# Kernel optimization log

Measured on AMD Instinct MI355X. Metric: run time of the kernel, lower is better.

## Reference

```python
import jax, jax.numpy as jnp
import numpy as np

N_RAYS = 65536
S_UNIFORM = 256          # 2 * n_samples coarse samples per ray
N_IMP = 128              # importance samples per ray
TRUNCATION = 2.0 / 512.0 * 4.0  # default in sdf2weights


def raw2weights_occupancy(raw):
    # raw2outputs_nerf_color with occupancy=True
    alpha = jax.nn.sigmoid(10.0 * raw)  # [N, S]
    trans = jnp.cumprod(
        jnp.concatenate([jnp.ones_like(alpha[:, :1]), 1.0 - alpha + 1e-10], axis=-1),
        axis=-1,
    )[:, :-1]
    return alpha, alpha * trans


def sample_pdf_det(bins, weights, n_samples):
    # bins: [N, M], weights: [N, M-1]; deterministic (det=True) inverse-CDF sampling
    w = weights + 1e-5
    pdf = w / jnp.sum(w, axis=-1, keepdims=True)
    cdf = jnp.cumsum(pdf, axis=-1)
    cdf = jnp.concatenate([jnp.zeros_like(cdf[..., :1]), cdf], axis=-1)  # [N, M]
    u = jnp.linspace(0.0, 1.0, n_samples, dtype=cdf.dtype)
    u = jnp.broadcast_to(u, cdf.shape[:-1] + (n_samples,))               # [N, n]
    inds = jax.vmap(lambda c, uu: jnp.searchsorted(c, uu, side='right'))(cdf, u)
    below = jnp.maximum(inds - 1, 0)
    above = jnp.minimum(inds, cdf.shape[-1] - 1)
    cdf_b = jnp.take_along_axis(cdf, below, axis=-1)
    cdf_a = jnp.take_along_axis(cdf, above, axis=-1)
    bins_b = jnp.take_along_axis(bins, below, axis=-1)
    bins_a = jnp.take_along_axis(bins, above, axis=-1)
    denom = cdf_a - cdf_b
    denom = jnp.where(denom < 1e-5, jnp.ones_like(denom), denom)
    t = (u - cdf_b) / denom
    return bins_b + t * (bins_a - bins_b)


def sdf2weights(sdf, z_vals, truncation=TRUNCATION, sc_factor=1.0):
    alpha = jax.nn.sigmoid(sdf / truncation) * jax.nn.sigmoid(-sdf / truncation)
    signs = sdf[:, 1:] * sdf[:, :-1]
    sign_mask = jnp.where(signs < 0.0, 1.0, 0.0)
    inds = jnp.argmax(sign_mask, axis=1)[:, None]              # first zero-crossing
    z_min = jnp.take_along_axis(z_vals, inds, axis=1)          # [N, 1]
    trunc_mask = jnp.where(z_vals < z_min + sc_factor * truncation, 1.0, 0.0)
    alpha = alpha * trunc_mask
    weights = alpha / (jnp.sum(alpha, axis=-1, keepdims=True) + 1e-8)
    return weights


def setup_inputs() -> dict:
    key = jax.random.key(0)
    k1, k2, k3, k4 = jax.random.split(key, 4)
    occ = jax.random.normal(k1, (N_RAYS, S_UNIFORM), dtype=jnp.float32)
    # monotonically increasing depths in [0.1, 4.1)
    z_vals_u = jnp.sort(
        jax.random.uniform(k2, (N_RAYS, S_UNIFORM), dtype=jnp.float32) * 4.0 + 0.1,
        axis=-1,
    )
    sdf = jax.random.normal(k3, (N_RAYS, N_IMP), dtype=jnp.float32) * 0.05
    rgbs = jax.random.uniform(k4, (N_RAYS, N_IMP, 3), dtype=jnp.float32)
    return {"occ": occ, "z_vals_u": z_vals_u, "sdf": sdf, "rgbs": rgbs}


def reference(occ, z_vals_u, sdf, rgbs):
    # 1) coarse occupancy compositing -> weights
    _, w_u = raw2weights_occupancy(occ)
    # 2) inverse-CDF importance sampling over midpoints (detached, as in gen_samples)
    z_mid = 0.5 * (z_vals_u[..., 1:] + z_vals_u[..., :-1])
    z_samples = jax.lax.stop_gradient(sample_pdf_det(z_mid, w_u[..., 1:-1], N_IMP))
    # 3) TSDF weights at importance samples
    weights = sdf2weights(sdf, z_samples)
    # 4) composite
    rgb_map = jnp.clip(jnp.sum(weights[..., None] * rgbs, axis=-2), 0.0, 1.0)  # [N,3]
    depth_map = jnp.sum(weights * z_samples, axis=-1)                          # [N]
    return jnp.concatenate([rgb_map, depth_map[:, None], weights], axis=-1)    # [N, 4+N_IMP]
```

## Files before the change

kernel.cpp:

```cpp
#include <hip/hip_runtime.h>

#define S_U 256
#define N_IMP 128
#define OUT_STRIDE (4 + N_IMP)
#define TRUNC 0.015625f
#define WPB 4
#define INV127 (1.0f / 127.0f)

template <int CTRL, int ROWM>
__device__ __forceinline__ float dppf(float identity, float x) {
    return __int_as_float(__builtin_amdgcn_update_dpp(
        __float_as_int(identity), __float_as_int(x), CTRL, ROWM, 0xf, false));
}

__device__ __forceinline__ float wscan_add(float x) {
    x += dppf<0x111, 0xf>(0.f, x);
    x += dppf<0x112, 0xf>(0.f, x);
    x += dppf<0x114, 0xf>(0.f, x);
    x += dppf<0x118, 0xf>(0.f, x);
    x += dppf<0x142, 0xa>(0.f, x);
    x += dppf<0x143, 0xc>(0.f, x);
    return x;
}

__device__ __forceinline__ float wscan_mul(float x) {
    x *= dppf<0x111, 0xf>(1.f, x);
    x *= dppf<0x112, 0xf>(1.f, x);
    x *= dppf<0x114, 0xf>(1.f, x);
    x *= dppf<0x118, 0xf>(1.f, x);
    x *= dppf<0x142, 0xa>(1.f, x);
    x *= dppf<0x143, 0xc>(1.f, x);
    return x;
}

__device__ __forceinline__ int wscan_min(int x) {
    const int I = 0x7fffffff;
    x = min(x, __builtin_amdgcn_update_dpp(I, x, 0x111, 0xf, 0xf, false));
    x = min(x, __builtin_amdgcn_update_dpp(I, x, 0x112, 0xf, 0xf, false));
    x = min(x, __builtin_amdgcn_update_dpp(I, x, 0x114, 0xf, 0xf, false));
    x = min(x, __builtin_amdgcn_update_dpp(I, x, 0x118, 0xf, 0xf, false));
    x = min(x, __builtin_amdgcn_update_dpp(I, x, 0x142, 0xa, 0xf, false));
    x = min(x, __builtin_amdgcn_update_dpp(I, x, 0x143, 0xc, 0xf, false));
    return x;
}

__device__ __forceinline__ int k_of(float c) {
    int k = (int)ceilf(c * 127.0f);
    k = min(max(k, 0), 128);
    if (k > 0 && c <= (float)(k - 1) * INV127) --k;
    else if (k < 128 && !(c <= (float)k * INV127)) ++k;
    return k;
}

__global__ __launch_bounds__(256) void tsdf_render_kernel(
    const float* __restrict__ occ,
    const float* __restrict__ zvals,
    const float* __restrict__ sdf,
    const float* __restrict__ rgbs,
    float* __restrict__ out)
{
    const int lane = threadIdx.x & 63;
    const int wv   = threadIdx.x >> 6;
    const int ray  = blockIdx.x * WPB + wv;

    __shared__ __align__(16) float2 s_pair[WPB][S_U];
    __shared__ int s_below[WPB][N_IMP];

    const float4 o4 = ((const float4*)(occ   + (size_t)ray * S_U))[lane];
    const float4 z4 = ((const float4*)(zvals + (size_t)ray * S_U))[lane];
    const float2 sd2 = ((const float2*)(sdf + (size_t)ray * N_IMP))[lane];
    const float2* rg = (const float2*)(rgbs + (size_t)ray * (N_IMP * 3)) + lane * 3;
    const float2 p0 = rg[0];
    const float2 p1 = rg[1];
    const float2 p2 = rg[2];

    float a0 = 1.0f / (1.0f + __expf(-10.0f * o4.x));
    float a1 = 1.0f / (1.0f + __expf(-10.0f * o4.y));
    float a2 = 1.0f / (1.0f + __expf(-10.0f * o4.z));
    float a3 = 1.0f / (1.0f + __expf(-10.0f * o4.w));
    float t0 = 1.0f - a0 + 1e-10f;
    float t1 = 1.0f - a1 + 1e-10f;
    float t2 = 1.0f - a2 + 1e-10f;
    float t3 = 1.0f - a3 + 1e-10f;
    float pp0 = t0, pp1 = pp0 * t1, pp2 = pp1 * t2, pp3 = pp2 * t3;
    float ip = wscan_mul(pp3);
    float pbase = __shfl_up(ip, 1);
    if (lane == 0) pbase = 1.0f;

    float w0 = a0 * pbase;
    float w1 = a1 * pbase * pp0;
    float w2 = a2 * pbase * pp1;
    float w3 = a3 * pbase * pp2;

    float v0 = (lane > 0)  ? w0 + 1e-5f : 0.0f;
    float v1 = w1 + 1e-5f;
    float v2 = w2 + 1e-5f;
    float v3 = (lane < 63) ? w3 + 1e-5f : 0.0f;
    float s0 = v0, s1 = s0 + v1, s2 = s1 + v2, s3 = s2 + v3;
    float is = wscan_add(s3);
    float total = __shfl(is, 63);
    float sbase = __shfl_up(is, 1);
    if (lane == 0) sbase = 0.0f;
    float invt = 1.0f / total;

    float c0 = (sbase + s0) * invt;
    float c1 = (sbase + s1) * invt;
    float c2 = (sbase + s2) * invt;
    float c3 = (sbase + s3) * invt;

    float znext = __shfl_down(z4.x, 1);
    float zm0 = 0.5f * (z4.x + z4.y);
    float zm1 = 0.5f * (z4.y + z4.z);
    float zm2 = 0.5f * (z4.z + z4.w);
    float zm3 = 0.5f * (z4.w + znext);

    float2* pr = s_pair[wv];
    *(float4*)&pr[lane * 4 + 0] = make_float4(c0, zm0, c1, zm1);
    *(float4*)&pr[lane * 4 + 2] = make_float4(c2, zm2, c3, zm3);

    int k0 = k_of(c0), k1 = k_of(c1), k2 = k_of(c2), k3 = k_of(c3);
    int kn = __shfl_down(k0, 1);
    if (lane == 63) { k3 = 128; kn = 128; }
    int base = lane * 4;
    int* bel = s_below[wv];
    for (int j = k0; j < k1; ++j) bel[j] = base;
    for (int j = k1; j < k2; ++j) bel[j] = base + 1;
    for (int j = k2; j < k3; ++j) bel[j] = base + 2;
    for (int j = k3; j < kn; ++j) bel[j] = base + 3;

    __builtin_amdgcn_wave_barrier();

    int jj0 = 2 * lane, jj1 = 2 * lane + 1;
    int b0 = bel[jj0], b1 = bel[jj1];
    float2 pb0 = pr[b0];
    float2 pa0 = pr[min(b0 + 1, 254)];
    float2 pb1 = pr[b1];
    float2 pa1 = pr[min(b1 + 1, 254)];

    float u0 = (float)jj0 * INV127;
    float u1 = (float)jj1 * INV127;
    float d0 = pa0.x - pb0.x; d0 = (d0 < 1e-5f) ? 1.0f : d0;
    float d1 = pa1.x - pb1.x; d1 = (d1 < 1e-5f) ? 1.0f : d1;
    float zs0 = pb0.y + ((u0 - pb0.x) / d0) * (pa0.y - pb0.y);
    float zs1 = pb1.y + ((u1 - pb1.x) / d1) * (pa1.y - pb1.y);

    float sn = __shfl_down(sd2.x, 1);
    int c = 0x7fffffff;
    if (sd2.x * sd2.y < 0.0f)                 c = 2 * lane;
    else if (lane < 63 && sd2.y * sn < 0.0f)  c = 2 * lane + 1;
    c = wscan_min(c);
    int ci = __shfl(c, 63);
    if (ci == 0x7fffffff) ci = 0;
    float zca = __shfl(zs0, ci >> 1);
    float zcb = __shfl(zs1, ci >> 1);
    float z_min = (ci & 1) ? zcb : zca;

    float x0 = sd2.x * (1.0f / TRUNC);
    float x1 = sd2.y * (1.0f / TRUNC);
    float al0 = 1.0f / (2.0f + __expf(x0) + __expf(-x0));
    float al1 = 1.0f / (2.0f + __expf(x1) + __expf(-x1));
    float zlim = z_min + TRUNC;
    if (!(zs0 < zlim)) al0 = 0.0f;
    if (!(zs1 < zlim)) al1 = 0.0f;

    float sA = wscan_add(al0 + al1);
    float sR = wscan_add(al0 * p0.x + al1 * p1.y);
    float sG = wscan_add(al0 * p0.y + al1 * p2.x);
    float sB = wscan_add(al0 * p1.x + al1 * p2.y);
    float sD = wscan_add(al0 * zs0  + al1 * zs1);

    float asum = __shfl(sA, 63);
    float inv_s = 1.0f / (asum + 1e-8f);

    float* ob = out + (size_t)ray * OUT_STRIDE;
    ((float2*)(ob + 4))[lane] = make_float2(al0 * inv_s, al1 * inv_s);
    if (lane == 63) {
        float inv63 = 1.0f / (sA + 1e-8f);
        ob[0] = fminf(fmaxf(sR * inv63, 0.0f), 1.0f);
        ob[1] = fminf(fmaxf(sG * inv63, 0.0f), 1.0f);
        ob[2] = fminf(fmaxf(sB * inv63, 0.0f), 1.0f);
        ob[3] = sD * inv63;
    }
}

extern "C" void kernel_launch(void* const* d_in, const int* in_sizes, int n_in,
                              void* d_out, int out_size, void* d_ws, size_t ws_size,
                              hipStream_t stream) {
    const float* occ  = (const float*)d_in[0];
    const float* z    = (const float*)d_in[1];
    const float* sdf  = (const float*)d_in[2];
    const float* rgbs = (const float*)d_in[3];
    float* out = (float*)d_out;
    const int n_rays = in_sizes[0] / S_U;
    hipLaunchKernelGGL(tsdf_render_kernel, dim3(n_rays / WPB), dim3(256), 0, stream,
                       occ, z, sdf, rgbs, out);
}
```

Baseline: 269.4 us.

## Replace divergent searchsorted fill loops with merge-path flag scan

Replaces the per-lane variable-length loops that write below-indices for each u sample with a merge-style approach. Each CDF point marks its merged position in a shared flag array, a wave prefix sum over those flags gives ranks, and each lane writes the below index for the u slots it owns. This is meant to remove warp divergence and load imbalance when many samples fall into a few bins. In exchange it adds extra LDS traffic, zeroing work, an integer scan and extra shared memory, which may lower occupancy.

After: 271.1 us. No clear change (+0.6%).

```diff
diff --git a/kernel.cpp b/kernel.cpp
--- a/kernel.cpp
+++ b/kernel.cpp
@@ -6,6 +6,7 @@
 #define TRUNC 0.015625f
 #define WPB 4
 #define INV127 (1.0f / 127.0f)
+#define MERGE_N 384
 
 template <int CTRL, int ROWM>
 __device__ __forceinline__ float dppf(float identity, float x) {
@@ -30,6 +31,16 @@
     x *= dppf<0x118, 0xf>(1.f, x);
     x *= dppf<0x142, 0xa>(1.f, x);
     x *= dppf<0x143, 0xc>(1.f, x);
+    return x;
+}
+
+__device__ __forceinline__ int wscan_add_i(int x) {
+    x += __builtin_amdgcn_update_dpp(0, x, 0x111, 0xf, 0xf, false);
+    x += __builtin_amdgcn_update_dpp(0, x, 0x112, 0xf, 0xf, false);
+    x += __builtin_amdgcn_update_dpp(0, x, 0x114, 0xf, 0xf, false);
+    x += __builtin_amdgcn_update_dpp(0, x, 0x118, 0xf, 0xf, false);
+    x += __builtin_amdgcn_update_dpp(0, x, 0x142, 0xa, 0xf, false);
+    x += __builtin_amdgcn_update_dpp(0, x, 0x143, 0xc, 0xf, false);
     return x;
 }
 
@@ -64,6 +75,7 @@
     const int ray  = blockIdx.x * WPB + wv;
 
     __shared__ __align__(16) float2 s_pair[WPB][S_U];
+    __shared__ __align__(16) int s_A[WPB][MERGE_N];
     __shared__ int s_below[WPB][N_IMP];
 
     const float4 o4 = ((const float4*)(occ   + (size_t)ray * S_U))[lane];
@@ -73,6 +85,10 @@
     const float2 p0 = rg[0];
     const float2 p1 = rg[1];
     const float2 p2 = rg[2];
+
+    int4* Az = (int4*)s_A[wv];
+    Az[lane] = make_int4(0, 0, 0, 0);
+    if (lane < 32) Az[64 + lane] = make_int4(0, 0, 0, 0);
 
     float a0 = 1.0f / (1.0f + __expf(-10.0f * o4.x));
     float a1 = 1.0f / (1.0f + __expf(-10.0f * o4.y));
@@ -119,26 +135,47 @@
     *(float4*)&pr[lane * 4 + 2] = make_float4(c2, zm2, c3, zm3);
 
     int k0 = k_of(c0), k1 = k_of(c1), k2 = k_of(c2), k3 = k_of(c3);
-    int kn = __shfl_down(k0, 1);
-    if (lane == 63) { k3 = 128; kn = 128; }
     int base = lane * 4;
+    int* Aw = s_A[wv];
+    __builtin_amdgcn_wave_barrier();
+    Aw[base + 0 + k0] = 1;
+    Aw[base + 1 + k1] = 1;
+    Aw[base + 2 + k2] = 1;
+    if (base + 3 < 255) Aw[base + 3 + k3] = 1;
+    __builtin_amdgcn_wave_barrier();
+
+    const int2 r0 = *(const int2*)&Aw[6 * lane + 0];
+    const int2 r1 = *(const int2*)&Aw[6 * lane + 2];
+    const int2 r2 = *(const int2*)&Aw[6 * lane + 4];
+    int q0 = r0.x, q1 = r0.y, q2 = r1.x, q3 = r1.y, q4 = r2.x, q5 = r2.y;
+    int e1 = q0, e2 = e1 + q1, e3 = e2 + q2, e4 = e3 + q3, e5 = e4 + q4;
+    int tot = e5 + q5;
+    int incl = wscan_add_i(tot);
+    int sb = __shfl_up(incl, 1);
+    if (lane == 0) sb = 0;
+
     int* bel = s_below[wv];
-    for (int j = k0; j < k1; ++j) bel[j] = base;
-    for (int j = k1; j < k2; ++j) bel[j] = base + 1;
-    for (int j = k2; j < k3; ++j) bel[j] = base + 2;
-    for (int j = k3; j < kn; ++j) bel[j] = base + 3;
-
+    int pbase6 = 6 * lane;
+    {
+        int Sx, j;
+        Sx = sb;      j = pbase6 + 0 - Sx; if (!q0 && j < 128) bel[j] = Sx - 1;
+        Sx = sb + e1; j = pbase6 + 1 - Sx; if (!q1 && j < 128) bel[j] = Sx - 1;
+        Sx = sb + e2; j = pbase6 + 2 - Sx; if (!q2 && j < 128) bel[j] = Sx - 1;
+        Sx = sb + e3; j = pbase6 + 3 - Sx; if (!q3 && j < 128) bel[j] = Sx - 1;
+        Sx = sb + e4; j = pbase6 + 4 - Sx; if (!q4 && j < 128) bel[j] = Sx - 1;
+        Sx = sb + e5; j = pbase6 + 5 - Sx; if (!q5 && j < 128) bel[j] = Sx - 1;
+    }
     __builtin_amdgcn_wave_barrier();
 
-    int jj0 = 2 * lane, jj1 = 2 * lane + 1;
-    int b0 = bel[jj0], b1 = bel[jj1];
+    const int2 bb = *(const int2*)&bel[2 * lane];
+    int b0 = bb.x, b1 = bb.y;
     float2 pb0 = pr[b0];
     float2 pa0 = pr[min(b0 + 1, 254)];
     float2 pb1 = pr[b1];
     float2 pa1 = pr[min(b1 + 1, 254)];
 
-    float u0 = (float)jj0 * INV127;
-    float u1 = (float)jj1 * INV127;
+    float u0 = (float)(2 * lane)     * INV127;
+    float u1 = (float)(2 * lane + 1) * INV127;
     float d0 = pa0.x - pb0.x; d0 = (d0 < 1e-5f) ? 1.0f : d0;
     float d1 = pa1.x - pb1.x; d1 = (d1 < 1e-5f) ? 1.0f : d1;
     float zs0 = pb0.y + ((u0 - pb0.x) / d0) * (pa0.y - pb0.y);
```
